# Kernel optimization log

Hardware: AMD Instinct MI355X
Metric: run time of the kernel (lower is better)

The kernel has to match this reference:

```python
import jax, jax.numpy as jnp
import numpy as np

D_MODEL = 1024
NUM_HEADS = 16
HEAD_DIM = D_MODEL // NUM_HEADS


def setup_inputs() -> dict:
    key = jax.random.key(0)
    ks = jax.random.split(key, 11)
    B, S, D = 2, 2048, D_MODEL
    scale = 1.0 / np.sqrt(D)
    inp = {
        "query": jax.random.normal(ks[0], (B, S, D), jnp.float32),
        "key": jax.random.normal(ks[1], (B, S, D), jnp.float32),
        "value": jax.random.normal(ks[2], (B, S, D), jnp.float32),
        "Wq": jax.random.normal(ks[3], (D, D), jnp.float32) * scale,
        "bq": jnp.zeros((D,), jnp.float32),
        "Wk": jax.random.normal(ks[4], (D, D), jnp.float32) * scale,
        "bk": jnp.zeros((D,), jnp.float32),
        "Wv": jax.random.normal(ks[5], (D, D), jnp.float32) * scale,
        "bv": jnp.zeros((D,), jnp.float32),
        "Wo": jax.random.normal(ks[6], (D, D), jnp.float32) * scale,
        "bo": jnp.zeros((D,), jnp.float32),
    }
    return inp


def reference(query, key, value, Wq, bq, Wk, bk, Wv, bv, Wo, bo):
    B, S, D = query.shape
    H, hd = NUM_HEADS, HEAD_DIM
    # linear projections (x @ W^T + b, torch nn.Linear convention)
    Q = query @ Wq.T + bq
    K = key @ Wk.T + bk
    V = value @ Wv.T + bv
    # split heads: [B, S, H, hd] -> [B, H, S, hd]
    Q = Q.reshape(B, S, H, hd).transpose(0, 2, 1, 3)
    K = K.reshape(B, S, H, hd).transpose(0, 2, 1, 3)
    V = V.reshape(B, S, H, hd).transpose(0, 2, 1, 3)
    # scaled dot-product attention (explicit, non-flash)
    scores = jnp.einsum("bhqd,bhkd->bhqk", Q, K) / jnp.sqrt(jnp.float32(hd)).astype(Q.dtype)
    attn = jax.nn.softmax(scores, axis=-1)
    out = jnp.einsum("bhqk,bhkd->bhqd", attn, V)
    # merge heads: [B, H, S, hd] -> [B, S, D]
    out = out.transpose(0, 2, 1, 3).reshape(B, S, D)
    return out @ Wo.T + bo
```

## Files before the change

kernel.cpp:

```cpp
#include <hip/hip_runtime.h>
#include <hip/hip_bf16.h>


constexpr int D_MODEL = 1024;
constexpr int S_LEN   = 2048;
constexpr int BATCH   = 2;
constexpr int NH      = 16;
constexpr int HD      = 64;
constexpr int ROWS    = BATCH * S_LEN;

typedef __attribute__((ext_vector_type(8))) short short8;
typedef __attribute__((ext_vector_type(4))) float float4a;

static __device__ __forceinline__ unsigned short f2bf(float f) {
  union { float f; unsigned u; } v{f};
  unsigned r = v.u + 0x7FFFu + ((v.u >> 16) & 1u);
  return (unsigned short)(r >> 16);
}

static __device__ __forceinline__ void async16(const void* g, void* l) {
  __builtin_amdgcn_global_load_lds(
      (const __attribute__((address_space(1))) unsigned int*)g,
      (__attribute__((address_space(3))) unsigned int*)l, 16, 0, 0);
}

struct ConvArgs { const float* s[7]; unsigned short* d[7]; int n[7]; };

__global__ __launch_bounds__(256) void convert_bf16(ConvArgs a) {
  const int which = blockIdx.y;
  const int i = (blockIdx.x * 256 + threadIdx.x) * 8;
  if (i >= a.n[which]) return;
  const float4* s = (const float4*)(a.s[which] + i);
  float4 x = s[0], y = s[1];
  unsigned short t[8] = {f2bf(x.x), f2bf(x.y), f2bf(x.z), f2bf(x.w),
                         f2bf(y.x), f2bf(y.y), f2bf(y.z), f2bf(y.w)};
  *(short8*)(a.d[which] + i) = *(short8*)t;
}

template <int MODE, int BM>
static __device__ __forceinline__ void gemm_body(
    const unsigned short* __restrict__ A, const unsigned short* __restrict__ W,
    const float* __restrict__ bias, void* __restrict__ Yv, float scale,
    unsigned short* As, unsigned short* Bs, unsigned short* Tb) {
  constexpr int NT = (BM == 128) ? 4 : 2;
  const int tid = threadIdx.x;
  const int w = tid >> 6, lane = tid & 63;
  const int l15 = lane & 15, quad = lane >> 4;
  const int row0 = blockIdx.x * BM, col0 = blockIdx.y * 128;
  const int wm = (BM == 128) ? (w & 1) * 64 : 0;
  const int wn = (BM == 128) ? (w >> 1) * 64 : w * 32;

  float4a acc[4][NT];
#pragma unroll
  for (int i = 0; i < 4; i++)
#pragma unroll
    for (int j = 0; j < NT; j++) acc[i][j] = (float4a){0.f, 0.f, 0.f, 0.f};

  const int swA = (quad + (wm >> 1) + (l15 >> 1)) & 3;
  const int swB = (quad + (wn >> 1) + (l15 >> 1)) & 3;

  for (int kt = 0; kt < D_MODEL; kt += 32) {
    __syncthreads();
#pragma unroll
    for (int j = 0; j < 2; j++) {
      const int i = w * 2 + j;
      const int r = i * 16 + (lane >> 2);
      const int c = ((lane & 3) - (r >> 1)) & 3;
      async16(W + (size_t)(col0 + r) * D_MODEL + kt + c * 8, (char*)Bs + i * 1024);
    }
    if constexpr (BM == 128) {
#pragma unroll
      for (int j = 0; j < 2; j++) {
        const int i = w * 2 + j;
        const int r = i * 16 + (lane >> 2);
        const int c = ((lane & 3) - (r >> 1)) & 3;
        async16(A + (size_t)(row0 + r) * D_MODEL + kt + c * 8, (char*)As + i * 1024);
      }
    } else {
      const int r = w * 16 + (lane >> 2);
      const int c = ((lane & 3) - (r >> 1)) & 3;
      async16(A + (size_t)(row0 + r) * D_MODEL + kt + c * 8, (char*)As + w * 1024);
    }
    __syncthreads();

    short8 af[4], bf[NT];
#pragma unroll
    for (int mt = 0; mt < 4; mt++) {
      const int r = wm + mt * 16 + l15;
      af[mt] = *(const short8*)&As[(r * 4 + swA) * 8];
    }
#pragma unroll
    for (int nt = 0; nt < NT; nt++) {
      const int r = wn + nt * 16 + l15;
      bf[nt] = *(const short8*)&Bs[(r * 4 + swB) * 8];
    }
#pragma unroll
    for (int mt = 0; mt < 4; mt++)
#pragma unroll
      for (int nt = 0; nt < NT; nt++)
        acc[mt][nt] = __builtin_amdgcn_mfma_f32_16x16x32_bf16(af[mt], bf[nt], acc[mt][nt], 0, 0, 0);
  }

  int cols[NT];
  float bvs[NT];
#pragma unroll
  for (int nt = 0; nt < NT; nt++) {
    cols[nt] = col0 + wn + nt * 16 + l15;
    bvs[nt]  = bias[cols[nt]] * ((MODE == 0) ? scale : 1.0f);
  }

  if constexpr (MODE == 0) {
    unsigned short* Y = (unsigned short*)Yv;
#pragma unroll
    for (int mt = 0; mt < 4; mt++)
#pragma unroll
      for (int r = 0; r < 4; r++) {
        const int m = row0 + wm + mt * 16 + quad * 4 + r;
        const int bb = m >> 11, s = m & 2047;
#pragma unroll
        for (int nt = 0; nt < NT; nt++) {
          const int h = cols[nt] >> 6, d = cols[nt] & 63;
          Y[(((size_t)(bb * NH + h)) * S_LEN + s) * HD + d] =
              f2bf(acc[mt][nt][r] * scale + bvs[nt]);
        }
      }
  } else if constexpr (MODE == 2) {
    unsigned short* T = Tb + w * 64 * 64;
#pragma unroll
    for (int mt = 0; mt < 4; mt++)
#pragma unroll
      for (int r = 0; r < 4; r++) {
        const int sl = mt * 16 + quad * 4 + r;
        const int cch = sl >> 3;
#pragma unroll
        for (int nt = 0; nt < NT; nt++) {
          const int dl = cols[nt] - col0 - wn;
          const int slot = cch ^ (dl & 7);
          T[dl * 64 + slot * 8 + (sl & 7)] = f2bf(acc[mt][nt][r] + bvs[nt]);
        }
      }
    asm volatile("s_waitcnt lgkmcnt(0)" ::: "memory");
    unsigned short* Y = (unsigned short*)Yv;
#pragma unroll
    for (int j = 0; j < 8; j++) {
      const int cid = j * 64 + lane;
      const int dl = cid >> 3;
      const int c  = cid & 7;
      const int slot = c ^ (dl & 7);
      short8 v = *(const short8*)&T[dl * 64 + slot * 8];
      const int col = col0 + wn + dl;
      const int h = col >> 6, d = col & 63;
      const int m = row0 + wm + c * 8;
      const int bb = m >> 11, s = m & 2047;
      *(short8*)&Y[(((size_t)(bb * NH + h)) * HD + d) * S_LEN + s] = v;
    }
  } else {
    float* Y = (float*)Yv;
#pragma unroll
    for (int mt = 0; mt < 4; mt++)
#pragma unroll
      for (int r = 0; r < 4; r++) {
        const int m = row0 + wm + mt * 16 + quad * 4 + r;
#pragma unroll
        for (int nt = 0; nt < NT; nt++)
          Y[(size_t)m * D_MODEL + cols[nt]] = acc[mt][nt][r] + bvs[nt];
      }
  }
}

__global__ __launch_bounds__(256) void gemm_qkv(
    const unsigned short* xq, const unsigned short* xk, const unsigned short* xv,
    const unsigned short* wq, const unsigned short* wk, const unsigned short* wv,
    const float* bq, const float* bk, const float* bv,
    unsigned short* Q, unsigned short* K, unsigned short* Vt) {
  __shared__ unsigned short As[128 * 32];
  __shared__ unsigned short Bs[128 * 32];
  __shared__ unsigned short Tb[4 * 64 * 64];
  const int z = blockIdx.z;
  if (z == 0)      gemm_body<0, 128>(xq, wq, bq, Q,  0.125f, As, Bs, Tb);
  else if (z == 1) gemm_body<0, 128>(xk, wk, bk, K,  1.0f,   As, Bs, Tb);
  else             gemm_body<2, 128>(xv, wv, bv, Vt, 1.0f,   As, Bs, Tb);
}

__global__ __launch_bounds__(256) void gemm_o(const unsigned short* o16, const unsigned short* wo,
                                              const float* bo, float* out) {
  __shared__ unsigned short As[64 * 32];
  __shared__ unsigned short Bs[128 * 32];
  gemm_body<3, 64>(o16, wo, bo, out, 1.0f, As, Bs, nullptr);
}

__global__ __launch_bounds__(256) void attn_kernel(
    const unsigned short* __restrict__ Qh, const unsigned short* __restrict__ Kh,
    const unsigned short* __restrict__ Vt, float* __restrict__ Op,
    float* __restrict__ Lp) {
  const int qb = blockIdx.x;
  const int h  = blockIdx.y;
  const int bb = blockIdx.z >> 1, sp = blockIdx.z & 1;
  const int tid = threadIdx.x;
  const int w = tid >> 6, lane = tid & 63;
  const int l15 = lane & 15, quad = lane >> 4;

  __shared__ unsigned short Ks[64 * 64];
  __shared__ unsigned short Vs[64 * 64];
  __shared__ unsigned short Ps[4][32][72];

  const size_t bh = (size_t)(bb * NH + h);
  const unsigned short* Qp = Qh + bh * S_LEN * HD;
  const unsigned short* Kp = Kh + bh * S_LEN * HD;
  const unsigned short* Vp = Vt + bh * (size_t)HD * S_LEN;

  short8 qf[2][2];
#pragma unroll
  for (int qnt = 0; qnt < 2; qnt++)
#pragma unroll
    for (int c = 0; c < 2; c++)
      qf[qnt][c] = *(const short8*)(Qp + (size_t)(qb * 128 + w * 32 + qnt * 16 + l15) * HD +
                                    c * 32 + quad * 8);

  float4a Oacc[2][4];
#pragma unroll
  for (int a = 0; a < 2; a++)
#pragma unroll
    for (int b = 0; b < 4; b++) Oacc[a][b] = (float4a){0.f, 0.f, 0.f, 0.f};
  float lp[2] = {0.f, 0.f};

  const int sw0 = (quad + l15) & 7;
  const int sw1 = (quad + 4 + l15) & 7;

  for (int kb = sp * 1024; kb < sp * 1024 + 1024; kb += 64) {
    __syncthreads();
#pragma unroll
    for (int j = 0; j < 2; j++) {
      const int i = w * 2 + j;
      const int r = i * 8 + (lane >> 3);
      const int c = ((lane & 7) - r) & 7;
      async16(Kp + (size_t)(kb + r) * HD + c * 8, (char*)Ks + i * 1024);
      async16(Vp + (size_t)r * S_LEN + kb + c * 8, (char*)Vs + i * 1024);
    }
    __syncthreads();

#pragma unroll
    for (int mt = 0; mt < 4; mt++) {
      const int rb = (mt * 16 + l15) * 8;
      short8 a0 = *(const short8*)&Ks[(rb + sw0) * 8];
      short8 a1 = *(const short8*)&Ks[(rb + sw1) * 8];
#pragma unroll
      for (int qnt = 0; qnt < 2; qnt++) {
        float4a s = (float4a){0.f, 0.f, 0.f, 0.f};
        s = __builtin_amdgcn_mfma_f32_16x16x32_bf16(a0, qf[qnt][0], s, 0, 0, 0);
        s = __builtin_amdgcn_mfma_f32_16x16x32_bf16(a1, qf[qnt][1], s, 0, 0, 0);
        const float p0 = __expf(s[0]), p1 = __expf(s[1]);
        const float p2 = __expf(s[2]), p3 = __expf(s[3]);
        lp[qnt] += (p0 + p1) + (p2 + p3);
        uint2 pk;
        pk.x = (unsigned)f2bf(p0) | ((unsigned)f2bf(p1) << 16);
        pk.y = (unsigned)f2bf(p2) | ((unsigned)f2bf(p3) << 16);
        *(uint2*)&Ps[w][qnt * 16 + l15][mt * 16 + quad * 4] = pk;
      }
    }
    asm volatile("s_waitcnt lgkmcnt(0)" ::: "memory");

#pragma unroll
    for (int c = 0; c < 2; c++) {
      short8 pa0 = *(const short8*)&Ps[w][l15][c * 32 + quad * 8];
      short8 pa1 = *(const short8*)&Ps[w][16 + l15][c * 32 + quad * 8];
      const int vsw = (c * 4 + quad + l15) & 7;
#pragma unroll
      for (int nt = 0; nt < 4; nt++) {
        short8 vb = *(const short8*)&Vs[((nt * 16 + l15) * 8 + vsw) * 8];
        Oacc[0][nt] = __builtin_amdgcn_mfma_f32_16x16x32_bf16(pa0, vb, Oacc[0][nt], 0, 0, 0);
        Oacc[1][nt] = __builtin_amdgcn_mfma_f32_16x16x32_bf16(pa1, vb, Oacc[1][nt], 0, 0, 0);
      }
    }
  }

#pragma unroll
  for (int qnt = 0; qnt < 2; qnt++) {
    lp[qnt] += __shfl_xor(lp[qnt], 16);
    lp[qnt] += __shfl_xor(lp[qnt], 32);
  }
  if (quad == 0) {
#pragma unroll
    for (int qnt = 0; qnt < 2; qnt++) {
      const int q = qb * 128 + w * 32 + qnt * 16 + l15;
      Lp[(size_t)sp * ROWS * NH + ((size_t)bb * S_LEN + q) * NH + h] = lp[qnt];
    }
  }

  float* Ob = Op + (size_t)sp * ROWS * D_MODEL;
#pragma unroll
  for (int qnt = 0; qnt < 2; qnt++) {
#pragma unroll
    for (int reg = 0; reg < 4; reg++) {
      const int q = qb * 128 + w * 32 + qnt * 16 + quad * 4 + reg;
      float* orow = Ob + ((size_t)bb * S_LEN + q) * D_MODEL + h * HD;
#pragma unroll
      for (int nt = 0; nt < 4; nt++)
        orow[nt * 16 + l15] = Oacc[qnt][nt][reg];
    }
  }
}

__global__ __launch_bounds__(256) void merge_kernel(const float* __restrict__ Op,
                                                    const float* __restrict__ Lp,
                                                    unsigned short* __restrict__ obuf) {
  const int e = (blockIdx.x * 256 + threadIdx.x) * 8;
  const int row = e >> 10, h = (e & 1023) >> 6;
  const float l = Lp[(size_t)row * NH + h] + Lp[(size_t)ROWS * NH + (size_t)row * NH + h];
  const float rinv = 1.0f / l;
  const float4* p0 = (const float4*)(Op + e);
  const float4* p1 = (const float4*)(Op + (size_t)ROWS * D_MODEL + e);
  float4 a = p0[0], b = p0[1], c = p1[0], d = p1[1];
  unsigned short t[8] = {
      f2bf((a.x + c.x) * rinv), f2bf((a.y + c.y) * rinv),
      f2bf((a.z + c.z) * rinv), f2bf((a.w + c.w) * rinv),
      f2bf((b.x + d.x) * rinv), f2bf((b.y + d.y) * rinv),
      f2bf((b.z + d.z) * rinv), f2bf((b.w + d.w) * rinv)};
  *(short8*)(obuf + e) = *(short8*)t;
}

extern "C" void kernel_launch(void* const* d_in, const int* in_sizes, int n_in,
                              void* d_out, int out_size, void* d_ws, size_t ws_size,
                              hipStream_t stream) {
  const float* query = (const float*)d_in[0];
  const float* key   = (const float*)d_in[1];
  const float* value = (const float*)d_in[2];
  const float* Wq = (const float*)d_in[3];
  const float* bq = (const float*)d_in[4];
  const float* Wk = (const float*)d_in[5];
  const float* bk = (const float*)d_in[6];
  const float* Wv = (const float*)d_in[7];
  const float* bv = (const float*)d_in[8];
  const float* Wo = (const float*)d_in[9];
  const float* bo = (const float*)d_in[10];
  float* out = (float*)d_out;

  char* ws = (char*)d_ws;
  const size_t MB = 1024 * 1024;
  unsigned short* xq16 = (unsigned short*)(ws + 0 * MB);
  unsigned short* xk16 = (unsigned short*)(ws + 8 * MB);
  unsigned short* xv16 = (unsigned short*)(ws + 16 * MB);
  unsigned short* wq16 = (unsigned short*)(ws + 24 * MB);
  unsigned short* wk16 = (unsigned short*)(ws + 26 * MB);
  unsigned short* wv16 = (unsigned short*)(ws + 28 * MB);
  unsigned short* qbuf  = (unsigned short*)(ws + 32 * MB);
  unsigned short* kbuf  = (unsigned short*)(ws + 40 * MB);
  unsigned short* vtbuf = (unsigned short*)(ws + 48 * MB);
  unsigned short* wo16  = (unsigned short*)(ws + 56 * MB);
  float* Lp  = (float*)(ws + 58 * MB);
  float* Op  = (float*)(ws + 0 * MB);
  unsigned short* obuf = qbuf;

  ConvArgs ca;
  const int NX = ROWS * D_MODEL, NW = D_MODEL * D_MODEL;
  ca.s[0] = query; ca.d[0] = xq16; ca.n[0] = NX;
  ca.s[1] = key;   ca.d[1] = xk16; ca.n[1] = NX;
  ca.s[2] = value; ca.d[2] = xv16; ca.n[2] = NX;
  ca.s[3] = Wq;    ca.d[3] = wq16; ca.n[3] = NW;
  ca.s[4] = Wk;    ca.d[4] = wk16; ca.n[4] = NW;
  ca.s[5] = Wv;    ca.d[5] = wv16; ca.n[5] = NW;
  ca.s[6] = Wo;    ca.d[6] = wo16; ca.n[6] = NW;
  hipLaunchKernelGGL(convert_bf16, dim3(NX / 2048, 7), dim3(256), 0, stream, ca);

  dim3 gqkv(ROWS / 128, D_MODEL / 128, 3);
  hipLaunchKernelGGL(gemm_qkv, gqkv, dim3(256), 0, stream,
                     xq16, xk16, xv16, wq16, wk16, wv16, bq, bk, bv,
                     qbuf, kbuf, vtbuf);

  dim3 ga(S_LEN / 128, NH, BATCH * 2);
  hipLaunchKernelGGL(attn_kernel, ga, dim3(256), 0, stream, qbuf, kbuf, vtbuf, Op, Lp);

  hipLaunchKernelGGL(merge_kernel, dim3(ROWS * D_MODEL / 2048), dim3(256), 0, stream,
                     Op, Lp, obuf);

  dim3 go(ROWS / 64, D_MODEL / 128);
  hipLaunchKernelGGL(gemm_o, go, dim3(256), 0, stream, obuf, wo16, bo, out);
}
```

Baseline: 243.1 us.

## Store attention partials in bf16, use exp2 with folded log2e, MFMA row sums

The attention kernel now writes its unnormalized per-split outputs as bf16 instead of fp32, which halves the partial-output write and the merge kernel's read. The log2(e) factor is folded into the Q projection scale so the softmax can use the hardware exp2 directly. Row sums of P are now computed with an extra MFMA against a ones vector instead of VALU adds and cross-lane shuffles. Packed bf16 conversion uses a hardware builtin where one exists. The costs are extra MFMA work and lower precision in the partial outputs, and the row sum is now taken over the bf16-rounded P values.

```diff
diff --git a/kernel.cpp b/kernel.cpp
--- a/kernel.cpp
+++ b/kernel.cpp
@@ -18,6 +18,23 @@
   return (unsigned short)(r >> 16);
 }
 
+static __device__ __forceinline__ unsigned pack_bf16(float a, float b) {
+#if __has_builtin(__builtin_amdgcn_cvt_pk_bf16_f32)
+  typedef __attribute__((ext_vector_type(2))) __bf16 bf16x2;
+  union { bf16x2 v; unsigned u; } c;
+  c.v = __builtin_amdgcn_cvt_pk_bf16_f32(a, b);
+  return c.u;
+#else
+  return (unsigned)f2bf(a) | ((unsigned)f2bf(b) << 16);
+#endif
+}
+
+static __device__ __forceinline__ float bf2f(unsigned short u) {
+  union { unsigned u; float f; } v;
+  v.u = (unsigned)u << 16;
+  return v.f;
+}
+
 static __device__ __forceinline__ void async16(const void* g, void* l) {
   __builtin_amdgcn_global_load_lds(
       (const __attribute__((address_space(1))) unsigned int*)g,
@@ -32,8 +49,8 @@
   if (i >= a.n[which]) return;
   const float4* s = (const float4*)(a.s[which] + i);
   float4 x = s[0], y = s[1];
-  unsigned short t[8] = {f2bf(x.x), f2bf(x.y), f2bf(x.z), f2bf(x.w),
-                         f2bf(y.x), f2bf(y.y), f2bf(y.z), f2bf(y.w)};
+  unsigned t[4] = {pack_bf16(x.x, x.y), pack_bf16(x.z, x.w),
+                   pack_bf16(y.x, y.y), pack_bf16(y.z, y.w)};
   *(short8*)(a.d[which] + i) = *(short8*)t;
 }
 
@@ -177,7 +194,7 @@
   __shared__ unsigned short Bs[128 * 32];
   __shared__ unsigned short Tb[4 * 64 * 64];
   const int z = blockIdx.z;
-  if (z == 0)      gemm_body<0, 128>(xq, wq, bq, Q,  0.125f, As, Bs, Tb);
+  if (z == 0)      gemm_body<0, 128>(xq, wq, bq, Q,  0.125f * 1.44269504f, As, Bs, Tb);
   else if (z == 1) gemm_body<0, 128>(xk, wk, bk, K,  1.0f,   As, Bs, Tb);
   else             gemm_body<2, 128>(xv, wv, bv, Vt, 1.0f,   As, Bs, Tb);
 }
@@ -191,7 +208,7 @@
 
 __global__ __launch_bounds__(256) void attn_kernel(
     const unsigned short* __restrict__ Qh, const unsigned short* __restrict__ Kh,
-    const unsigned short* __restrict__ Vt, float* __restrict__ Op,
+    const unsigned short* __restrict__ Vt, unsigned short* __restrict__ Op,
     float* __restrict__ Lp) {
   const int qb = blockIdx.x;
   const int h  = blockIdx.y;
@@ -217,12 +234,15 @@
       qf[qnt][c] = *(const short8*)(Qp + (size_t)(qb * 128 + w * 32 + qnt * 16 + l15) * HD +
                                     c * 32 + quad * 8);
 
+  unsigned short ob[8] = {0x3F80, 0x3F80, 0x3F80, 0x3F80, 0x3F80, 0x3F80, 0x3F80, 0x3F80};
+  const short8 ones = *(short8*)ob;
+
   float4a Oacc[2][4];
 #pragma unroll
   for (int a = 0; a < 2; a++)
 #pragma unroll
     for (int b = 0; b < 4; b++) Oacc[a][b] = (float4a){0.f, 0.f, 0.f, 0.f};
-  float lp[2] = {0.f, 0.f};
+  float4a Lacc[2] = {(float4a){0.f, 0.f, 0.f, 0.f}, (float4a){0.f, 0.f, 0.f, 0.f}};
 
   const int sw0 = (quad + l15) & 7;
   const int sw1 = (quad + 4 + l15) & 7;
@@ -249,12 +269,9 @@
         float4a s = (float4a){0.f, 0.f, 0.f, 0.f};
         s = __builtin_amdgcn_mfma_f32_16x16x32_bf16(a0, qf[qnt][0], s, 0, 0, 0);
         s = __builtin_amdgcn_mfma_f32_16x16x32_bf16(a1, qf[qnt][1], s, 0, 0, 0);
-        const float p0 = __expf(s[0]), p1 = __expf(s[1]);
-        const float p2 = __expf(s[2]), p3 = __expf(s[3]);
-        lp[qnt] += (p0 + p1) + (p2 + p3);
         uint2 pk;
-        pk.x = (unsigned)f2bf(p0) | ((unsigned)f2bf(p1) << 16);
-        pk.y = (unsigned)f2bf(p2) | ((unsigned)f2bf(p3) << 16);
+        pk.x = pack_bf16(__builtin_amdgcn_exp2f(s[0]), __builtin_amdgcn_exp2f(s[1]));
+        pk.y = pack_bf16(__builtin_amdgcn_exp2f(s[2]), __builtin_amdgcn_exp2f(s[3]));
         *(uint2*)&Ps[w][qnt * 16 + l15][mt * 16 + quad * 4] = pk;
       }
     }
@@ -264,6 +281,8 @@
     for (int c = 0; c < 2; c++) {
       short8 pa0 = *(const short8*)&Ps[w][l15][c * 32 + quad * 8];
       short8 pa1 = *(const short8*)&Ps[w][16 + l15][c * 32 + quad * 8];
+      Lacc[0] = __builtin_amdgcn_mfma_f32_16x16x32_bf16(pa0, ones, Lacc[0], 0, 0, 0);
+      Lacc[1] = __builtin_amdgcn_mfma_f32_16x16x32_bf16(pa1, ones, Lacc[1], 0, 0, 0);
       const int vsw = (c * 4 + quad + l15) & 7;
 #pragma unroll
       for (int nt = 0; nt < 4; nt++) {
@@ -274,48 +293,46 @@
     }
   }
 
-#pragma unroll
-  for (int qnt = 0; qnt < 2; qnt++) {
-    lp[qnt] += __shfl_xor(lp[qnt], 16);
-    lp[qnt] += __shfl_xor(lp[qnt], 32);
-  }
-  if (quad == 0) {
-#pragma unroll
-    for (int qnt = 0; qnt < 2; qnt++) {
-      const int q = qb * 128 + w * 32 + qnt * 16 + l15;
-      Lp[(size_t)sp * ROWS * NH + ((size_t)bb * S_LEN + q) * NH + h] = lp[qnt];
-    }
-  }
-
-  float* Ob = Op + (size_t)sp * ROWS * D_MODEL;
+  if (l15 == 0) {
+#pragma unroll
+    for (int qnt = 0; qnt < 2; qnt++)
+#pragma unroll
+      for (int reg = 0; reg < 4; reg++) {
+        const int q = qb * 128 + w * 32 + qnt * 16 + quad * 4 + reg;
+        Lp[(size_t)sp * ROWS * NH + ((size_t)bb * S_LEN + q) * NH + h] = Lacc[qnt][reg];
+      }
+  }
+
+  unsigned short* Ob = Op + (size_t)sp * ROWS * D_MODEL;
 #pragma unroll
   for (int qnt = 0; qnt < 2; qnt++) {
 #pragma unroll
     for (int reg = 0; reg < 4; reg++) {
       const int q = qb * 128 + w * 32 + qnt * 16 + quad * 4 + reg;
-      float* orow = Ob + ((size_t)bb * S_LEN + q) * D_MODEL + h * HD;
+      unsigned short* orow = Ob + ((size_t)bb * S_LEN + q) * D_MODEL + h * HD;
 #pragma unroll
       for (int nt = 0; nt < 4; nt++)
-        orow[nt * 16 + l15] = Oacc[qnt][nt][reg];
-    }
-  }
-}
-
-__global__ __launch_bounds__(256) void merge_kernel(const float* __restrict__ Op,
+        orow[nt * 16 + l15] = f2bf(Oacc[qnt][nt][reg]);
+    }
+  }
+}
+
+__global__ __launch_bounds__(256) void merge_kernel(const unsigned short* __restrict__ Op,
                                                     const float* __restrict__ Lp,
                                                     unsigned short* __restrict__ obuf) {
   const int e = (blockIdx.x * 256 + threadIdx.x) * 8;
   const int row = e >> 10, h = (e & 1023) >> 6;
   const float l = Lp[(size_t)row * NH + h] + Lp[(size_t)ROWS * NH + (size_t)row * NH + h];
   const float rinv = 1.0f / l;
-  const float4* p0 = (const float4*)(Op + e);
-  const float4* p1 = (const float4*)(Op + (size_t)ROWS * D_MODEL + e);
-  float4 a = p0[0], b = p0[1], c = p1[0], d = p1[1];
-  unsigned short t[8] = {
-      f2bf((a.x + c.x) * rinv), f2bf((a.y + c.y) * rinv),
-      f2bf((a.z + c.z) * rinv), f2bf((a.w + c.w) * rinv),
-      f2bf((b.x + d.x) * rinv), f2bf((b.y + d.y) * rinv),
-      f2bf((b.z + d.z) * rinv), f2bf((b.w + d.w) * rinv)};
+  short8 a = *(const short8*)(Op + e);
+  short8 b = *(const short8*)(Op + (size_t)ROWS * D_MODEL + e);
+  unsigned t[4];
+#pragma unroll
+  for (int i = 0; i < 4; i++) {
+    const float v0 = (bf2f((unsigned short)a[2 * i]) + bf2f((unsigned short)b[2 * i])) * rinv;
+    const float v1 = (bf2f((unsigned short)a[2 * i + 1]) + bf2f((unsigned short)b[2 * i + 1])) * rinv;
+    t[i] = pack_bf16(v0, v1);
+  }
   *(short8*)(obuf + e) = *(short8*)t;
 }
 
@@ -348,7 +365,7 @@
   unsigned short* vtbuf = (unsigned short*)(ws + 48 * MB);
   unsigned short* wo16  = (unsigned short*)(ws + 56 * MB);
   float* Lp  = (float*)(ws + 58 * MB);
-  float* Op  = (float*)(ws + 0 * MB);
+  unsigned short* Op = (unsigned short*)(ws + 0 * MB);
   unsigned short* obuf = qbuf;
 
   ConvArgs ca;
```

Result: faster. 236.1 us (-2.9%).
